# Optimization experiments

Hardware: AMD Instinct MI355X
Metric: run time of the kernel (lower is better)

Reference implementation:

```python
import jax, jax.numpy as jnp
import numpy as np

N = 50000      # number of atoms/nodes
D = 32         # atom_dim == units (pad_length = 0)
E = 300000     # number of bonds/edges
BD = 16        # bond_dim
STEPS = 4      # message passing steps


def setup_inputs() -> dict:
    key = jax.random.key(0)
    ks = jax.random.split(key, 8)
    atom_features = jax.random.normal(ks[0], (N, D), dtype=jnp.float32)
    bond_features = jax.random.uniform(ks[1], (E, BD), dtype=jnp.float32)
    pair_indices = jax.random.randint(ks[2], (E, 2), 0, N, dtype=jnp.int32)
    # EdgeNetwork kernel: xavier_uniform on [bond_dim, atom_dim*atom_dim]
    s = float(np.sqrt(6.0 / (BD + D * D)))
    kernel = jax.random.uniform(ks[3], (BD, D * D), dtype=jnp.float32, minval=-s, maxval=s)
    bias = jnp.zeros((D * D,), dtype=jnp.float32)
    # torch.nn.GRUCell init: U(-1/sqrt(H), 1/sqrt(H)), H = D (pad_length = 0)
    stdv = float(1.0 / np.sqrt(D))
    W_ih = jax.random.uniform(ks[4], (3 * D, D), dtype=jnp.float32, minval=-stdv, maxval=stdv)
    W_hh = jax.random.uniform(ks[5], (3 * D, D), dtype=jnp.float32, minval=-stdv, maxval=stdv)
    b_ih = jax.random.uniform(ks[6], (3 * D,), dtype=jnp.float32, minval=-stdv, maxval=stdv)
    b_hh = jax.random.uniform(ks[7], (3 * D,), dtype=jnp.float32, minval=-stdv, maxval=stdv)
    return {
        "atom_features": atom_features,
        "bond_features": bond_features,
        "pair_indices": pair_indices,
        "kernel": kernel,
        "bias": bias,
        "W_ih": W_ih,
        "W_hh": W_hh,
        "b_ih": b_ih,
        "b_hh": b_hh,
    }


def _gru_cell(x, h, W_ih, W_hh, b_ih, b_hh):
    # torch.nn.GRUCell math, gates stacked as (r, z, n)
    gi = x @ W_ih.T + b_ih  # [N, 3D]
    gh = h @ W_hh.T + b_hh  # [N, 3D]
    i_r, i_z, i_n = jnp.split(gi, 3, axis=-1)
    h_r, h_z, h_n = jnp.split(gh, 3, axis=-1)
    r = jax.nn.sigmoid(i_r + h_r)
    z = jax.nn.sigmoid(i_z + h_z)
    n = jnp.tanh(i_n + r * h_n)
    return (1.0 - z) * n + z * h


def reference(atom_features, bond_features, pair_indices, kernel, bias, W_ih, W_hh, b_ih, b_hh):
    # pad_length = units - atom_dim = 0, so no padding needed.
    W = kernel.reshape(BD, D, D)   # per-bond-feature DxD transforms
    Bm = bias.reshape(D, D)        # bias as DxD matrix applied to neighbor feats
    dst = pair_indices[:, 0]       # aggregation (index_add) target
    src = pair_indices[:, 1]       # gathered neighbor

    h = atom_features
    for _ in range(STEPS):
        nbr = h[src]  # [E, D] gather
        # transformed[e, i] = sum_j (bond[e] @ kernel + bias)[i, j] * nbr[e, j]
        msg = jnp.einsum('eb,bij,ej->ei', bond_features, W, nbr) + nbr @ Bm.T
        agg = jax.ops.segment_sum(msg, dst, num_segments=N)  # scatter-add
        h = _gru_cell(agg, h, W_ih, W_hh, b_ih, b_hh)
    return h
```

## Files before the change

### kernel.cpp

```cpp
#include <hip/hip_runtime.h>
#include <math.h>

#define N_ATOMS 50000
#define D 32
#define E_EDGES 300000
#define BD 16
#define SW 544
#define SCAN_BLOCKS ((N_ATOMS + 255) / 256)
#define GRU_TILE 8
#define GRU_NT (N_ATOMS / GRU_TILE)

#define NB 64
#define FBLOCKS ((N_ATOMS + NB - 1) / NB)
#define EBF 512

__device__ __forceinline__ float sigmoidf_(float x) {
    return 1.0f / (1.0f + __expf(-x));
}


__global__ void k_build_wt(const float* __restrict__ kern,
                           const float* __restrict__ bias,
                           float* __restrict__ WTj) {
    int idx = blockIdx.x * 256 + threadIdx.x;
    if (idx >= 32 * SW) return;
    int j = idx / SW;
    int r = idx - j * SW;
    int b = r >> 5, i = r & 31;
    WTj[idx] = (b < BD) ? kern[b * 1024 + i * 32 + j] : bias[i * 32 + j];
}

__global__ void k_hist(const int* __restrict__ pair, int* __restrict__ deg) {
    int e = blockIdx.x * 256 + threadIdx.x;
    if (e < E_EDGES) atomicAdd(&deg[pair[2 * e + 1]], 1);
}

__global__ void k_scan1(const int* __restrict__ deg, int* __restrict__ offs,
                        int* __restrict__ bsums) {
    __shared__ int sm[256];
    int t = threadIdx.x, gid = blockIdx.x * 256 + t;
    int v = (gid < N_ATOMS) ? deg[gid] : 0;
    sm[t] = v;
    __syncthreads();
    for (int off = 1; off < 256; off <<= 1) {
        int x = (t >= off) ? sm[t - off] : 0;
        __syncthreads();
        sm[t] += x;
        __syncthreads();
    }
    if (gid < N_ATOMS) offs[gid] = sm[t] - v;
    if (t == 255) bsums[blockIdx.x] = sm[255];
}

__global__ void k_scan2(const int* __restrict__ bsums, int* __restrict__ boffs, int nb) {
    __shared__ int sm[256];
    int t = threadIdx.x;
    int v = (t < nb) ? bsums[t] : 0;
    sm[t] = v;
    __syncthreads();
    for (int off = 1; off < 256; off <<= 1) {
        int x = (t >= off) ? sm[t - off] : 0;
        __syncthreads();
        sm[t] += x;
        __syncthreads();
    }
    if (t < nb) boffs[t] = sm[t] - v;
}

__global__ void k_scan3(int* __restrict__ offs, const int* __restrict__ boffs) {
    int gid = blockIdx.x * 256 + threadIdx.x;
    if (gid < N_ATOMS) offs[gid] += boffs[blockIdx.x];
}

__global__ void k_scatter(const int* __restrict__ pair, const int* __restrict__ offs,
                          int* __restrict__ cursor, int2* __restrict__ sedge) {
    int e = blockIdx.x * 256 + threadIdx.x;
    if (e >= E_EDGES) return;
    int d = pair[2 * e], s = pair[2 * e + 1];
    int pos = offs[s] + atomicAdd(&cursor[s], 1);
    sedge[pos] = make_int2(d, e);
}

__global__ __launch_bounds__(256, 2)
void k_fused(const float* __restrict__ h_in, float* __restrict__ agg,
             const float* __restrict__ bond, const float* __restrict__ WTj,
             const int* __restrict__ offs, const int* __restrict__ deg,
             const int2* __restrict__ sedge) {
    __shared__ float h_lds[NB][33];
    __shared__ float bond_s[EBF][BD];
    __shared__ int   dst_s[EBF];

    const int t = threadIdx.x;
    const int bbase = blockIdx.x * NB;
    const int i = t & 31;
    const int grp = t >> 5;
    const int nbase = bbase + grp * 8;
    const int hn0 = grp * 8;

#pragma unroll
    for (int k = 0; k < 8; ++k) {
        const int idx = t + 256 * k;
        const int n = idx >> 5, j = idx & 31;
        const int node = bbase + n;
        h_lds[n][j] = (node < N_ATOMS) ? h_in[(size_t)node * D + j] : 0.f;
    }

    int stv[8], env[8];
#pragma unroll
    for (int n = 0; n < 8; ++n) {
        const int node = nbase + n;
        const bool ok = (node < N_ATOMS);
        const int o = ok ? offs[node] : 0;
        stv[n] = o;
        env[n] = o + (ok ? deg[node] : 0);
    }
    __syncthreads();

    float y[8][17];
#pragma unroll
    for (int n = 0; n < 8; ++n)
#pragma unroll
        for (int b = 0; b < 17; ++b) y[n][b] = 0.f;

    for (int j = 0; j < 32; ++j) {
        float wv[17];
#pragma unroll
        for (int b = 0; b < 17; ++b)
            wv[b] = WTj[j * SW + b * 32 + i];
#pragma unroll
        for (int n = 0; n < 8; ++n) {
            const float hv = h_lds[hn0 + n][j];
#pragma unroll
            for (int b = 0; b < 17; ++b)
                y[n][b] = fmaf(wv[b], hv, y[n][b]);
        }
    }

    const int lastn = min(bbase + NB - 1, N_ATOMS - 1);
    const int bstart = offs[bbase];
    const int bend = offs[lastn] + deg[lastn];

    for (int ebase = bstart; ebase < bend; ebase += EBF) {
        const int ecnt = min(EBF, bend - ebase);
        const int nch = ecnt * 4;
        __syncthreads();
#pragma unroll
        for (int k2 = 0; k2 < 8; ++k2) {
            const int c = t + 256 * k2;
            if (c < nch) {
                const int2 se = sedge[ebase + (c >> 2)];
                if ((c & 3) == 0) dst_s[c >> 2] = se.x;
                ((float4*)bond_s)[c] =
                    *(const float4*)(bond + (size_t)se.y * BD + (c & 3) * 4);
            }
        }
        __syncthreads();
        const int elim = ebase + ecnt;
#pragma unroll
        for (int n = 0; n < 8; ++n) {
            const int s = max(stv[n], ebase);
            const int e = min(env[n], elim);
            for (int p = s; p < e; ++p) {
                const int l = p - ebase;
                const float4 b0 = *(const float4*)&bond_s[l][0];
                const float4 b1 = *(const float4*)&bond_s[l][4];
                const float4 b2 = *(const float4*)&bond_s[l][8];
                const float4 b3 = *(const float4*)&bond_s[l][12];
                float m = y[n][16];
                m = fmaf(b0.x, y[n][0],  m); m = fmaf(b0.y, y[n][1],  m);
                m = fmaf(b0.z, y[n][2],  m); m = fmaf(b0.w, y[n][3],  m);
                m = fmaf(b1.x, y[n][4],  m); m = fmaf(b1.y, y[n][5],  m);
                m = fmaf(b1.z, y[n][6],  m); m = fmaf(b1.w, y[n][7],  m);
                m = fmaf(b2.x, y[n][8],  m); m = fmaf(b2.y, y[n][9],  m);
                m = fmaf(b2.z, y[n][10], m); m = fmaf(b2.w, y[n][11], m);
                m = fmaf(b3.x, y[n][12], m); m = fmaf(b3.y, y[n][13], m);
                m = fmaf(b3.z, y[n][14], m); m = fmaf(b3.w, y[n][15], m);
                atomicAdd(&agg[(size_t)dst_s[l] * D + i], m);
            }
        }
    }
}

__global__ __launch_bounds__(256, 2)
void k_gru(const float* __restrict__ agg_g, const float* __restrict__ h_in,
           float* __restrict__ h_out,
           const float* __restrict__ Wih, const float* __restrict__ Whh,
           const float* __restrict__ bih, const float* __restrict__ bhh) {
    __shared__ float Wih_s[96][33];
    __shared__ float Whh_s[96][33];
    __shared__ float bih_s[96], bhh_s[96];
    __shared__ float x_lds[GRU_TILE][32];
    __shared__ float h_lds[GRU_TILE][32];

    const int t = threadIdx.x;

    for (int idx = t; idx < 96 * 32; idx += 256) {
        const int o = idx >> 5, jj = idx & 31;
        Wih_s[o][jj] = Wih[idx];
        Whh_s[o][jj] = Whh[idx];
    }
    if (t < 96) { bih_s[t] = bih[t]; bhh_s[t] = bhh[t]; }

    const int r = t >> 5;
    const int i = t & 31;
    const int stride = gridDim.x;

    int tile = blockIdx.x;
    float xr = 0.f, hr = 0.f;
    if (tile < GRU_NT) {
        xr = agg_g[tile * 256 + t];
        hr = h_in[tile * 256 + t];
    }
    for (; tile < GRU_NT; tile += stride) {
        ((float*)x_lds)[t] = xr;
        ((float*)h_lds)[t] = hr;
        __syncthreads();
        const int nxt = tile + stride;
        if (nxt < GRU_NT) {
            xr = agg_g[nxt * 256 + t];
            hr = h_in[nxt * 256 + t];
        }
        float gri = bih_s[i],      grh = bhh_s[i];
        float gzi = bih_s[32 + i], gzh = bhh_s[32 + i];
        float gni = bih_s[64 + i], gnh = bhh_s[64 + i];
#pragma unroll 8
        for (int jj = 0; jj < 32; ++jj) {
            const float xv = x_lds[r][jj];
            const float hv = h_lds[r][jj];
            gri = fmaf(Wih_s[i][jj],      xv, gri);
            gzi = fmaf(Wih_s[32 + i][jj], xv, gzi);
            gni = fmaf(Wih_s[64 + i][jj], xv, gni);
            grh = fmaf(Whh_s[i][jj],      hv, grh);
            gzh = fmaf(Whh_s[32 + i][jj], hv, gzh);
            gnh = fmaf(Whh_s[64 + i][jj], hv, gnh);
        }
        const float rg = sigmoidf_(gri + grh);
        const float zg = sigmoidf_(gzi + gzh);
        float xn = gni + rg * gnh;
        xn = fminf(fmaxf(xn, -15.f), 15.f);
        const float e2 = __expf(2.f * xn);
        const float ng = (e2 - 1.f) / (e2 + 1.f);
        h_out[tile * 256 + t] = (1.f - zg) * ng + zg * h_lds[r][i];
        __syncthreads();
    }
}

extern "C" void kernel_launch(void* const* d_in, const int* in_sizes, int n_in,
                              void* d_out, int out_size, void* d_ws, size_t ws_size,
                              hipStream_t stream) {
    const float* atom = (const float*)d_in[0];
    const float* bond = (const float*)d_in[1];
    const int*   pair = (const int*)d_in[2];
    const float* kern = (const float*)d_in[3];
    const float* bias = (const float*)d_in[4];
    const float* Wih  = (const float*)d_in[5];
    const float* Whh  = (const float*)d_in[6];
    const float* bih  = (const float*)d_in[7];
    const float* bhh  = (const float*)d_in[8];
    float* out = (float*)d_out;

    char* w = (char*)d_ws;
    auto alloc = [&](size_t bytes) {
        char* p = w;
        w += (bytes + 255) & ~size_t(255);
        return p;
    };
    float* hA     = (float*)alloc((size_t)N_ATOMS * D * 4);
    float* aggG   = (float*)alloc((size_t)N_ATOMS * D * 4);
    float* WTj    = (float*)alloc((size_t)32 * SW * 4);
    int*   deg    = (int*)alloc((size_t)N_ATOMS * 4);
    int*   offs   = (int*)alloc((size_t)N_ATOMS * 4);
    int*   cursor = (int*)alloc((size_t)N_ATOMS * 4);
    int*   bsums  = (int*)alloc(256 * 4);
    int*   boffs  = (int*)alloc(256 * 4);
    int2*  sedge  = (int2*)alloc((size_t)E_EDGES * 8);

    hipMemsetAsync(deg, 0, (size_t)N_ATOMS * 4, stream);
    hipMemsetAsync(cursor, 0, (size_t)N_ATOMS * 4, stream);

    k_build_wt<<<(32 * SW + 255) / 256, 256, 0, stream>>>(kern, bias, WTj);
    k_hist<<<(E_EDGES + 255) / 256, 256, 0, stream>>>(pair, deg);
    k_scan1<<<SCAN_BLOCKS, 256, 0, stream>>>(deg, offs, bsums);
    k_scan2<<<1, 256, 0, stream>>>(bsums, boffs, SCAN_BLOCKS);
    k_scan3<<<SCAN_BLOCKS, 256, 0, stream>>>(offs, boffs);
    k_scatter<<<(E_EDGES + 255) / 256, 256, 0, stream>>>(pair, offs, cursor, sedge);

    const float* hsrc = atom;
    float* hdst[4] = { hA, out, hA, out };
    for (int s = 0; s < 4; ++s) {
        hipMemsetAsync(aggG, 0, (size_t)N_ATOMS * D * 4, stream);
        k_fused<<<FBLOCKS, 256, 0, stream>>>(hsrc, aggG, bond, WTj, offs, deg, sedge);
        k_gru<<<2048, 256, 0, stream>>>(aggG, hsrc, hdst[s], Wih, Whh, bih, bhh);
        hsrc = hdst[s];
    }
}
```

Measured before the change: 514.4 us.

## Pre-permute bond features by source, stream edges directly, fold agg zeroing into GRU

```diff
diff --git a/kernel.cpp b/kernel.cpp
--- a/kernel.cpp
+++ b/kernel.cpp
@@ -10,9 +10,8 @@
 #define GRU_TILE 8
 #define GRU_NT (N_ATOMS / GRU_TILE)
 
-#define NB 64
+#define NB 32
 #define FBLOCKS ((N_ATOMS + NB - 1) / NB)
-#define EBF 512
 
 __device__ __forceinline__ float sigmoidf_(float x) {
     return 1.0f / (1.0f + __expf(-x));
@@ -72,43 +71,58 @@
     if (gid < N_ATOMS) offs[gid] += boffs[blockIdx.x];
 }
 
-__global__ void k_scatter(const int* __restrict__ pair, const int* __restrict__ offs,
-                          int* __restrict__ cursor, int2* __restrict__ sedge) {
+__global__ void k_scatter_perm(const int* __restrict__ pair, const int* __restrict__ offs,
+                               int* __restrict__ cursor, const float* __restrict__ bond,
+                               float* __restrict__ bond_perm, int* __restrict__ dst_perm) {
     int e = blockIdx.x * 256 + threadIdx.x;
     if (e >= E_EDGES) return;
     int d = pair[2 * e], s = pair[2 * e + 1];
     int pos = offs[s] + atomicAdd(&cursor[s], 1);
-    sedge[pos] = make_int2(d, e);
-}
+    dst_perm[pos] = d;
+    const float4* src4 = (const float4*)(bond + (size_t)e * BD);
+    float4* dst4 = (float4*)(bond_perm + (size_t)pos * BD);
+    dst4[0] = src4[0];
+    dst4[1] = src4[1];
+    dst4[2] = src4[2];
+    dst4[3] = src4[3];
+}
+
+#define EDGE_FMA(M, B0, B1, B2, B3, YN) do {            \
+    M = fmaf(B0.x, YN[0],  M); M = fmaf(B0.y, YN[1],  M); \
+    M = fmaf(B0.z, YN[2],  M); M = fmaf(B0.w, YN[3],  M); \
+    M = fmaf(B1.x, YN[4],  M); M = fmaf(B1.y, YN[5],  M); \
+    M = fmaf(B1.z, YN[6],  M); M = fmaf(B1.w, YN[7],  M); \
+    M = fmaf(B2.x, YN[8],  M); M = fmaf(B2.y, YN[9],  M); \
+    M = fmaf(B2.z, YN[10], M); M = fmaf(B2.w, YN[11], M); \
+    M = fmaf(B3.x, YN[12], M); M = fmaf(B3.y, YN[13], M); \
+    M = fmaf(B3.z, YN[14], M); M = fmaf(B3.w, YN[15], M); \
+} while (0)
 
 __global__ __launch_bounds__(256, 2)
 void k_fused(const float* __restrict__ h_in, float* __restrict__ agg,
-             const float* __restrict__ bond, const float* __restrict__ WTj,
-             const int* __restrict__ offs, const int* __restrict__ deg,
-             const int2* __restrict__ sedge) {
+             const float* __restrict__ bond_perm, const int* __restrict__ dst_perm,
+             const float* __restrict__ WTj,
+             const int* __restrict__ offs, const int* __restrict__ deg) {
     __shared__ float h_lds[NB][33];
-    __shared__ float bond_s[EBF][BD];
-    __shared__ int   dst_s[EBF];
 
     const int t = threadIdx.x;
     const int bbase = blockIdx.x * NB;
     const int i = t & 31;
     const int grp = t >> 5;
-    const int nbase = bbase + grp * 8;
-    const int hn0 = grp * 8;
-
-#pragma unroll
-    for (int k = 0; k < 8; ++k) {
+    const int hn0 = grp * 4;
+
+#pragma unroll
+    for (int k = 0; k < 4; ++k) {
         const int idx = t + 256 * k;
         const int n = idx >> 5, j = idx & 31;
         const int node = bbase + n;
         h_lds[n][j] = (node < N_ATOMS) ? h_in[(size_t)node * D + j] : 0.f;
     }
 
-    int stv[8], env[8];
-#pragma unroll
-    for (int n = 0; n < 8; ++n) {
-        const int node = nbase + n;
+    int stv[4], env[4];
+#pragma unroll
+    for (int n = 0; n < 4; ++n) {
+        const int node = bbase + hn0 + n;
         const bool ok = (node < N_ATOMS);
         const int o = ok ? offs[node] : 0;
         stv[n] = o;
@@ -116,9 +130,9 @@
     }
     __syncthreads();
 
-    float y[8][17];
-#pragma unroll
-    for (int n = 0; n < 8; ++n)
+    float y[4][17];
+#pragma unroll
+    for (int n = 0; n < 4; ++n)
 #pragma unroll
         for (int b = 0; b < 17; ++b) y[n][b] = 0.f;
 
@@ -128,7 +142,7 @@
         for (int b = 0; b < 17; ++b)
             wv[b] = WTj[j * SW + b * 32 + i];
 #pragma unroll
-        for (int n = 0; n < 8; ++n) {
+        for (int n = 0; n < 4; ++n) {
             const float hv = h_lds[hn0 + n][j];
 #pragma unroll
             for (int b = 0; b < 17; ++b)
@@ -136,53 +150,37 @@
         }
     }
 
-    const int lastn = min(bbase + NB - 1, N_ATOMS - 1);
-    const int bstart = offs[bbase];
-    const int bend = offs[lastn] + deg[lastn];
-
-    for (int ebase = bstart; ebase < bend; ebase += EBF) {
-        const int ecnt = min(EBF, bend - ebase);
-        const int nch = ecnt * 4;
-        __syncthreads();
-#pragma unroll
-        for (int k2 = 0; k2 < 8; ++k2) {
-            const int c = t + 256 * k2;
-            if (c < nch) {
-                const int2 se = sedge[ebase + (c >> 2)];
-                if ((c & 3) == 0) dst_s[c >> 2] = se.x;
-                ((float4*)bond_s)[c] =
-                    *(const float4*)(bond + (size_t)se.y * BD + (c & 3) * 4);
-            }
-        }
-        __syncthreads();
-        const int elim = ebase + ecnt;
-#pragma unroll
-        for (int n = 0; n < 8; ++n) {
-            const int s = max(stv[n], ebase);
-            const int e = min(env[n], elim);
-            for (int p = s; p < e; ++p) {
-                const int l = p - ebase;
-                const float4 b0 = *(const float4*)&bond_s[l][0];
-                const float4 b1 = *(const float4*)&bond_s[l][4];
-                const float4 b2 = *(const float4*)&bond_s[l][8];
-                const float4 b3 = *(const float4*)&bond_s[l][12];
-                float m = y[n][16];
-                m = fmaf(b0.x, y[n][0],  m); m = fmaf(b0.y, y[n][1],  m);
-                m = fmaf(b0.z, y[n][2],  m); m = fmaf(b0.w, y[n][3],  m);
-                m = fmaf(b1.x, y[n][4],  m); m = fmaf(b1.y, y[n][5],  m);
-                m = fmaf(b1.z, y[n][6],  m); m = fmaf(b1.w, y[n][7],  m);
-                m = fmaf(b2.x, y[n][8],  m); m = fmaf(b2.y, y[n][9],  m);
-                m = fmaf(b2.z, y[n][10], m); m = fmaf(b2.w, y[n][11], m);
-                m = fmaf(b3.x, y[n][12], m); m = fmaf(b3.y, y[n][13], m);
-                m = fmaf(b3.z, y[n][14], m); m = fmaf(b3.w, y[n][15], m);
-                atomicAdd(&agg[(size_t)dst_s[l] * D + i], m);
-            }
+#pragma unroll
+    for (int n = 0; n < 4; ++n) {
+        int p = stv[n];
+        const int e = env[n];
+        for (; p + 2 <= e; p += 2) {
+            const float4* bp0 = (const float4*)(bond_perm + (size_t)p * BD);
+            const float4* bp1 = (const float4*)(bond_perm + (size_t)(p + 1) * BD);
+            const int d0 = dst_perm[p];
+            const int d1 = dst_perm[p + 1];
+            const float4 a0 = bp0[0], a1 = bp0[1], a2 = bp0[2], a3 = bp0[3];
+            const float4 c0 = bp1[0], c1 = bp1[1], c2 = bp1[2], c3 = bp1[3];
+            float m0 = y[n][16];
+            float m1 = y[n][16];
+            EDGE_FMA(m0, a0, a1, a2, a3, y[n]);
+            EDGE_FMA(m1, c0, c1, c2, c3, y[n]);
+            atomicAdd(&agg[(size_t)d0 * D + i], m0);
+            atomicAdd(&agg[(size_t)d1 * D + i], m1);
+        }
+        if (p < e) {
+            const float4* bp0 = (const float4*)(bond_perm + (size_t)p * BD);
+            const int d0 = dst_perm[p];
+            const float4 a0 = bp0[0], a1 = bp0[1], a2 = bp0[2], a3 = bp0[3];
+            float m0 = y[n][16];
+            EDGE_FMA(m0, a0, a1, a2, a3, y[n]);
+            atomicAdd(&agg[(size_t)d0 * D + i], m0);
         }
     }
 }
 
 __global__ __launch_bounds__(256, 2)
-void k_gru(const float* __restrict__ agg_g, const float* __restrict__ h_in,
+void k_gru(float* __restrict__ agg_g, const float* __restrict__ h_in,
            float* __restrict__ h_out,
            const float* __restrict__ Wih, const float* __restrict__ Whh,
            const float* __restrict__ bih, const float* __restrict__ bhh) {
@@ -214,6 +212,7 @@
     for (; tile < GRU_NT; tile += stride) {
         ((float*)x_lds)[t] = xr;
         ((float*)h_lds)[t] = hr;
+        agg_g[tile * 256 + t] = 0.f;
         __syncthreads();
         const int nxt = tile + stride;
         if (nxt < GRU_NT) {
@@ -265,31 +264,34 @@
         w += (bytes + 255) & ~size_t(255);
         return p;
     };
-    float* hA     = (float*)alloc((size_t)N_ATOMS * D * 4);
-    float* aggG   = (float*)alloc((size_t)N_ATOMS * D * 4);
-    float* WTj    = (float*)alloc((size_t)32 * SW * 4);
-    int*   deg    = (int*)alloc((size_t)N_ATOMS * 4);
-    int*   offs   = (int*)alloc((size_t)N_ATOMS * 4);
-    int*   cursor = (int*)alloc((size_t)N_ATOMS * 4);
-    int*   bsums  = (int*)alloc(256 * 4);
-    int*   boffs  = (int*)alloc(256 * 4);
-    int2*  sedge  = (int2*)alloc((size_t)E_EDGES * 8);
+    float* hA        = (float*)alloc((size_t)N_ATOMS * D * 4);
+    float* aggG      = (float*)alloc((size_t)N_ATOMS * D * 4);
+    float* WTj       = (float*)alloc((size_t)32 * SW * 4);
+    int*   deg       = (int*)alloc((size_t)N_ATOMS * 4);
+    int*   offs      = (int*)alloc((size_t)N_ATOMS * 4);
+    int*   cursor    = (int*)alloc((size_t)N_ATOMS * 4);
+    int*   bsums     = (int*)alloc(256 * 4);
+    int*   boffs     = (int*)alloc(256 * 4);
+    int*   dst_perm  = (int*)alloc((size_t)E_EDGES * 4);
+    float* bond_perm = (float*)alloc((size_t)E_EDGES * BD * 4);
 
     hipMemsetAsync(deg, 0, (size_t)N_ATOMS * 4, stream);
     hipMemsetAsync(cursor, 0, (size_t)N_ATOMS * 4, stream);
+    hipMemsetAsync(aggG, 0, (size_t)N_ATOMS * D * 4, stream);
 
     k_build_wt<<<(32 * SW + 255) / 256, 256, 0, stream>>>(kern, bias, WTj);
     k_hist<<<(E_EDGES + 255) / 256, 256, 0, stream>>>(pair, deg);
     k_scan1<<<SCAN_BLOCKS, 256, 0, stream>>>(deg, offs, bsums);
     k_scan2<<<1, 256, 0, stream>>>(bsums, boffs, SCAN_BLOCKS);
     k_scan3<<<SCAN_BLOCKS, 256, 0, stream>>>(offs, boffs);
-    k_scatter<<<(E_EDGES + 255) / 256, 256, 0, stream>>>(pair, offs, cursor, sedge);
+    k_scatter_perm<<<(E_EDGES + 255) / 256, 256, 0, stream>>>(pair, offs, cursor,
+                                                              bond, bond_perm, dst_perm);
 
     const float* hsrc = atom;
     float* hdst[4] = { hA, out, hA, out };
     for (int s = 0; s < 4; ++s) {
-        hipMemsetAsync(aggG, 0, (size_t)N_ATOMS * D * 4, stream);
-        k_fused<<<FBLOCKS, 256, 0, stream>>>(hsrc, aggG, bond, WTj, offs, deg, sedge);
+        k_fused<<<FBLOCKS, 256, 0, stream>>>(hsrc, aggG, bond_perm, dst_perm,
+                                             WTj, offs, deg);
         k_gru<<<2048, 256, 0, stream>>>(aggG, hsrc, hdst[s], Wih, Whh, bih, bhh);
         hsrc = hdst[s];
     }
```

Measured after the change: 496.8 us. -3.4%, faster.
